# Kernel optimization log

Hardware: AMD Instinct MI355X
Metric: run time of the kernel (lower is better)

## Reference

```python
import jax, jax.numpy as jnp
import numpy as np

H = 1024      # hidden_size
NH = 16       # num_heads
HD = H // NH  # head_dim


def setup_inputs() -> dict:
    key = jax.random.key(0)
    ks = jax.random.split(key, 12)
    inp = {
        "query": jax.random.normal(ks[0], (4, 1024, H), dtype=jnp.float32),
        "key": jax.random.normal(ks[1], (4, 2048, H), dtype=jnp.float32),
        "value": jax.random.normal(ks[2], (4, 2048, H), dtype=jnp.float32),
        "key_padding_mask": jax.random.randint(ks[3], (4, 2048), 0, 2, dtype=jnp.int32),
        # learned parameters (torch Linear: y = x @ W.T + b); we store W already transposed
        "Wq": jax.random.normal(ks[4], (H, H), dtype=jnp.float32) * (1.0 / np.sqrt(H)),
        "bq": jnp.zeros((H,), dtype=jnp.float32),
        "Wk": jax.random.normal(ks[5], (H, H), dtype=jnp.float32) * (1.0 / np.sqrt(H)),
        "bk": jnp.zeros((H,), dtype=jnp.float32),
        "Wv": jax.random.normal(ks[6], (H, H), dtype=jnp.float32) * (1.0 / np.sqrt(H)),
        "bv": jnp.zeros((H,), dtype=jnp.float32),
        "Wo": jax.random.normal(ks[7], (H, H), dtype=jnp.float32) * (1.0 / np.sqrt(H)),
        "bo": jnp.zeros((H,), dtype=jnp.float32),
    }
    return inp


def reference(query, key, value, key_padding_mask, Wq, bq, Wk, bk, Wv, bv, Wo, bo):
    B, Sq, _ = query.shape
    Sk = key.shape[1]
    scaling = HD ** -0.5
    # projections -> [B, NH, S, HD]
    q = (query @ Wq + bq).reshape(B, Sq, NH, HD).transpose(0, 2, 1, 3)
    k = (key @ Wk + bk).reshape(B, Sk, NH, HD).transpose(0, 2, 1, 3)
    v = (value @ Wv + bv).reshape(B, Sk, NH, HD).transpose(0, 2, 1, 3)
    # scores [B, NH, Sq, Sk]
    scores = jnp.einsum("bhqd,bhkd->bhqk", q, k) * scaling
    # mask: positions where key_padding_mask == 0 are ignored
    scores = jnp.where((key_padding_mask == 0)[:, None, None, :], -jnp.inf, scores)
    attn = jax.nn.softmax(scores, axis=-1)
    # dropout is identity in eval mode
    out = jnp.einsum("bhqk,bhkd->bhqd", attn, v)
    out = out.transpose(0, 2, 1, 3).reshape(B, Sq, H)
    return out @ Wo + bo
```

## Files before the change

kernel.cpp:

```cpp
#include <hip/hip_runtime.h>
#include <hip/hip_fp16.h>
#include <math.h>

#define B_ 4
#define SQ 1024
#define SK 2048
#define HH 1024
#define NHEAD 16
#define HDIM 64

typedef _Float16 f16;
typedef __attribute__((ext_vector_type(8))) _Float16 f16x8;
typedef __attribute__((ext_vector_type(4))) _Float16 f16x4;
typedef __attribute__((ext_vector_type(4))) float f32x4;
typedef unsigned int u32;

#define GLOAD_LDS16(gp, lp) __builtin_amdgcn_global_load_lds( \
    (const __attribute__((address_space(1))) u32*)(gp),        \
    (__attribute__((address_space(3))) u32*)(lp), 16, 0, 0)
#define GLOAD_LDS4(gp, lp) __builtin_amdgcn_global_load_lds(  \
    (const __attribute__((address_space(1))) u32*)(gp),        \
    (__attribute__((address_space(3))) u32*)(lp), 4, 0, 0)

__global__ __launch_bounds__(256) void prep_k(
    const float* __restrict__ W0, const float* __restrict__ W1,
    const float* __restrict__ W2, const float* __restrict__ W3,
    const int* __restrict__ mask,
    f16* __restrict__ WT, float* __restrict__ pbias)
{
    __shared__ f16 t[64 * 80];
    const int bid = blockIdx.x, tid = threadIdx.x;
    if (bid < 1024) {
        int z = bid >> 8, idx = bid & 255;
        const float* W = z == 0 ? W0 : z == 1 ? W1 : z == 2 ? W2 : W3;
        f16* out = WT + (size_t)z * HH * HH;
        const int r0 = (idx >> 4) * 64, c0 = (idx & 15) * 64;
#pragma unroll
        for (int p = 0; p < 4; p++) {
            int s = p * 256 + tid;
            int row = s >> 4, u = s & 15;
            float4 a = *(const float4*)(W + (size_t)(r0 + row) * HH + c0 + u * 4);
            f16x4 vv;
            vv[0] = (f16)a.x; vv[1] = (f16)a.y; vv[2] = (f16)a.z; vv[3] = (f16)a.w;
            *(f16x4*)(t + row * 80 + u * 4) = vv;
        }
        __syncthreads();
#pragma unroll
        for (int p = 0; p < 2; p++) {
            int s = p * 256 + tid;
            int n = s >> 3, u = s & 7;
            f16x8 vv;
#pragma unroll
            for (int j = 0; j < 8; j++) vv[j] = t[(u * 8 + j) * 80 + n];
            *(f16x8*)(out + (size_t)(c0 + n) * HH + r0 + u * 8) = vv;
        }
    } else {
        int j = (bid - 1024) * 256 + tid;
        pbias[j] = mask[j] ? 0.f : -1e30f;
    }
}

template <int TM, int OUTMODE, int CASTA>
__device__ __forceinline__ void gemm_body(
    const void* Ain, const f16* __restrict__ BT,
    const float* __restrict__ bias, void* __restrict__ Cout,
    int bid, int nwg, f16* sA, f16* sB)
{
    const int tid = threadIdx.x, lane = tid & 63, w = tid >> 6;
    const int swz = (bid & 7) * (nwg >> 3) + (bid >> 3);
    const int m0 = (swz >> 3) * TM;
    const int n0 = (swz & 7) * 128;
    const int wr = w >> 1, wc = w & 1;
    const int ql = lane & 15, g = lane >> 4;
    const int N = 1024, K = 1024;
    const int MF = TM / 32;
    const int ABUF = TM * 32;
    f32x4 acc[TM / 32][4] = {};

    auto stage = [&](int buf, int k0) {
        if (CASTA) {
            const float* A32 = (const float*)Ain;
#pragma unroll
            for (int p = 0; p < TM / 64; p++) {
                int s = p * 256 + tid;
                int row = s >> 2, u = s & 3;
                const float* ap = A32 + (size_t)(m0 + row) * K + k0 + u * 8;
                float4 a0 = *(const float4*)ap;
                float4 a1 = *(const float4*)(ap + 4);
                f16x8 v;
                v[0] = (f16)a0.x; v[1] = (f16)a0.y; v[2] = (f16)a0.z; v[3] = (f16)a0.w;
                v[4] = (f16)a1.x; v[5] = (f16)a1.y; v[6] = (f16)a1.z; v[7] = (f16)a1.w;
                *(f16x8*)(sA + buf * ABUF + row * 32 + ((u ^ ((row >> 1) & 3)) * 8)) = v;
            }
        } else {
            const f16* A16 = (const f16*)Ain;
#pragma unroll
            for (int p = 0; p < TM / 64; p++) {
                int s = p * 256 + tid;
                int row = s >> 2, us = ((s & 3) ^ ((row >> 1) & 3)) * 8;
                GLOAD_LDS16(A16 + (size_t)(m0 + row) * K + k0 + us,
                            sA + buf * ABUF + (p * 256 + w * 64) * 8);
            }
        }
#pragma unroll
        for (int p = 0; p < 2; p++) {
            int s = p * 256 + tid;
            int row = s >> 2, us = ((s & 3) ^ ((row >> 1) & 3)) * 8;
            GLOAD_LDS16(BT + (size_t)(n0 + row) * K + k0 + us,
                        sB + buf * 4096 + (p * 256 + w * 64) * 8);
        }
    };

    stage(0, 0);
    int cur = 0;
    for (int k0 = 0; k0 < K; k0 += 32) {
        __syncthreads();
        if (k0 + 32 < K) stage(cur ^ 1, k0 + 32);
        f16x8 af[MF], bf[4];
#pragma unroll
        for (int m = 0; m < MF; m++) {
            int row = wr * (TM / 2) + m * 16 + ql;
            af[m] = *(const f16x8*)(sA + cur * ABUF + row * 32 + ((g ^ ((row >> 1) & 3)) * 8));
        }
#pragma unroll
        for (int n = 0; n < 4; n++) {
            int row = wc * 64 + n * 16 + ql;
            bf[n] = *(const f16x8*)(sB + cur * 4096 + row * 32 + ((g ^ ((row >> 1) & 3)) * 8));
        }
#pragma unroll
        for (int m = 0; m < MF; m++)
#pragma unroll
            for (int n = 0; n < 4; n++)
                acc[m][n] = __builtin_amdgcn_mfma_f32_16x16x32_f16(af[m], bf[n], acc[m][n], 0, 0, 0);
        cur ^= 1;
    }

    float bv[4];
#pragma unroll
    for (int n = 0; n < 4; n++) bv[n] = bias[n0 + wc * 64 + n * 16 + ql];
#pragma unroll
    for (int m = 0; m < MF; m++) {
        int row0 = m0 + wr * (TM / 2) + m * 16 + g * 4;
#pragma unroll
        for (int n = 0; n < 4; n++) {
            int col = n0 + wc * 64 + n * 16 + ql;
            if (OUTMODE == 2) {
                int bb = row0 >> 11, kk = row0 & 2047;
                int hh = col >> 6, dd = col & 63;
                f16x4 vv;
#pragma unroll
                for (int e = 0; e < 4; e++) vv[e] = (f16)(acc[m][n][e] + bv[n]);
                *(f16x4*)((f16*)Cout + ((size_t)(bb * NHEAD + hh) * HDIM + dd) * SK + kk) = vv;
            } else if (OUTMODE == 1) {
#pragma unroll
                for (int e = 0; e < 4; e++)
                    ((f16*)Cout)[(size_t)(row0 + e) * N + col] = (f16)(acc[m][n][e] + bv[n]);
            } else {
#pragma unroll
                for (int e = 0; e < 4; e++)
                    ((float*)Cout)[(size_t)(row0 + e) * N + col] = acc[m][n][e] + bv[n];
            }
        }
    }
}

__global__ __launch_bounds__(256) void qkv_gemm_k(
    const float* __restrict__ q, const float* __restrict__ k,
    const float* __restrict__ v, const f16* __restrict__ wT,
    const float* __restrict__ bq, const float* __restrict__ bk,
    const float* __restrict__ bv,
    f16* __restrict__ qp, f16* __restrict__ kp, f16* __restrict__ vt)
{
    __shared__ f16 sA[2 * 4096];
    __shared__ f16 sB[2 * 4096];
    const int bid = blockIdx.x;
    const size_t M1 = 1024 * 1024;
    if (bid < 512)
        gemm_body<64, 1, 1>(q, wT, bq, qp, bid, 512, sA, sB);
    else if (bid < 1024)
        gemm_body<128, 1, 1>(k, wT + M1, bk, kp, bid - 512, 512, sA, sB);
    else
        gemm_body<128, 2, 1>(v, wT + 2 * M1, bv, vt, bid - 1024, 512, sA, sB);
}

__global__ __launch_bounds__(256) void o_gemm_k(
    const f16* __restrict__ ctx, const f16* __restrict__ wT,
    const float* __restrict__ bo, float* __restrict__ out)
{
    __shared__ f16 sA[2 * 4096];
    __shared__ f16 sB[2 * 4096];
    gemm_body<64, 0, 0>(ctx, wT, bo, out, blockIdx.x, 512, sA, sB);
}

#define SC2 0.18033688f
#define THR2 11.5f

__global__ __launch_bounds__(512, 4) void attn_mfma_k(
    const f16* __restrict__ qp,
    const f16* __restrict__ kp,
    const f16* __restrict__ vt,
    const float* __restrict__ pbias,
    f16* __restrict__ ctx)
{
    const int flat = ((int)blockIdx.x & 7) * 64 + ((int)blockIdx.x >> 3);
    const int qt = flat & 7, h = (flat >> 3) & 15, b = flat >> 7;
    const int q0 = qt * 128;
    const int tid = threadIdx.x, lane = tid & 63, w = tid >> 6;
    const int ql = lane & 15, g = lane >> 4;

    __shared__ f16 ks[2 * 4096];
    __shared__ f16 vs[2 * 4096];
    __shared__ f16 plds[8][16 * 64];
    __shared__ float sbias[2][64];

    const f16* kbase = kp + (size_t)b * SK * HH + h * HDIM;
    const f16* vbase = vt + ((size_t)(b * NHEAD + h)) * HDIM * SK;
    const float* bbase = pbias + b * SK;

    f16x8 qf[2];
    {
        const f16* qb = qp + ((size_t)(b * SQ + q0 + w * 16 + ql)) * HH + h * HDIM + g * 8;
        qf[0] = *(const f16x8*)qb;
        qf[1] = *(const f16x8*)(qb + 32);
    }

    auto stageKV = [&](int buf, int kt) {
        int r = tid >> 3, ulg = ((tid & 7) ^ (r & 7)) * 8;
        GLOAD_LDS16(kbase + (size_t)(kt + r) * HH + ulg, ks + buf * 4096 + w * 512);
        GLOAD_LDS16(vbase + (size_t)r * SK + kt + ulg,   vs + buf * 4096 + w * 512);
        if (w == 0) GLOAD_LDS4(bbase + kt + lane, &sbias[buf][0]);
    };

    f32x4 oacc[4] = {};
    float mrun = -1e30f, lrun = 0.f;
    f16* pw = &plds[w][0];

    auto tile = [&](const f16* kb, const f16* vb, const float* sb,
                    bool pf_en, int pbuf, int pkt) {
        __syncthreads();
        if (pf_en) stageKV(pbuf, pkt);

        f32x4 sacc[4] = {};
        __builtin_amdgcn_s_setprio(1);
#pragma unroll
        for (int n = 0; n < 4; n++) {
            int key = n * 16 + ql;
#pragma unroll
            for (int df = 0; df < 2; df++) {
                int u = df * 4 + g;
                f16x8 kf = *(const f16x8*)(kb + key * 64 + ((u ^ (key & 7)) * 8));
                sacc[n] = __builtin_amdgcn_mfma_f32_16x16x32_f16(kf, qf[df], sacc[n], 0, 0, 0);
            }
        }
        __builtin_amdgcn_s_setprio(0);

        float sv[4][4];
        float mt = -1e30f;
#pragma unroll
        for (int n = 0; n < 4; n++) {
            float4 b4 = *(const float4*)&sb[n * 16 + g * 4];
            float barr[4] = {b4.x, b4.y, b4.z, b4.w};
#pragma unroll
            for (int e = 0; e < 4; e++) {
                float s = fmaf(sacc[n][e], SC2, barr[e]);
                sv[n][e] = s;
                mt = fmaxf(mt, s);
            }
        }
        mt = fmaxf(mt, __shfl_xor(mt, 16, 64));
        mt = fmaxf(mt, __shfl_xor(mt, 32, 64));

        if (__any(mt > mrun + THR2)) {
            float mnew = fmaxf(mrun, mt);
            float alpha = __builtin_amdgcn_exp2f(mrun - mnew);
            mrun = mnew;
            lrun *= alpha;
            float al[4];
#pragma unroll
            for (int e = 0; e < 4; e++) al[e] = __shfl(alpha, g * 4 + e, 64);
#pragma unroll
            for (int df = 0; df < 4; df++)
#pragma unroll
                for (int e = 0; e < 4; e++) oacc[df][e] *= al[e];
        }

        float tsum = 0.f;
#pragma unroll
        for (int n = 0; n < 4; n++) {
            float p0 = __builtin_amdgcn_exp2f(sv[n][0] - mrun);
            float p1 = __builtin_amdgcn_exp2f(sv[n][1] - mrun);
            float p2 = __builtin_amdgcn_exp2f(sv[n][2] - mrun);
            float p3 = __builtin_amdgcn_exp2f(sv[n][3] - mrun);
            tsum += (p0 + p1) + (p2 + p3);
            f16x4 pv4;
            pv4[0] = (f16)p0; pv4[1] = (f16)p1; pv4[2] = (f16)p2; pv4[3] = (f16)p3;
            *(f16x4*)(pw + ql * 64 + (((2 * n + (g >> 1)) ^ (ql & 7)) * 8) + (g & 1) * 4) = pv4;
        }
        tsum += __shfl_xor(tsum, 16, 64);
        tsum += __shfl_xor(tsum, 32, 64);
        lrun += tsum;

        __builtin_amdgcn_s_setprio(1);
#pragma unroll
        for (int t = 0; t < 2; t++) {
            f16x8 pf = *(const f16x8*)(pw + ql * 64 + (((t * 4 + g) ^ (ql & 7)) * 8));
#pragma unroll
            for (int df = 0; df < 4; df++) {
                int d = df * 16 + ql;
                int u = t * 4 + g;
                f16x8 vf = *(const f16x8*)(vb + d * 64 + ((u ^ (d & 7)) * 8));
                oacc[df] = __builtin_amdgcn_mfma_f32_16x16x32_f16(pf, vf, oacc[df], 0, 0, 0);
            }
        }
        __builtin_amdgcn_s_setprio(0);
    };

    stageKV(0, 0);
#pragma unroll 1
    for (int kt = 0; kt < SK; kt += 128) {
        tile(ks, vs, sbias[0], true, 1, kt + 64);
        tile(ks + 4096, vs + 4096, sbias[1], kt + 128 < SK, 0, kt + 128);
    }

    float linv[4];
#pragma unroll
    for (int e = 0; e < 4; e++) {
        float lv = __shfl(lrun, g * 4 + e, 64);
        linv[e] = 1.f / lv;
    }
    f16* ob = ctx + ((size_t)(b * SQ + q0 + w * 16)) * HH + h * HDIM;
#pragma unroll
    for (int df = 0; df < 4; df++)
#pragma unroll
        for (int e = 0; e < 4; e++)
            ob[(size_t)(g * 4 + e) * HH + df * 16 + ql] = (f16)(oacc[df][e] * linv[e]);
}

extern "C" void kernel_launch(void* const* d_in, const int* in_sizes, int n_in,
                              void* d_out, int out_size, void* d_ws, size_t ws_size,
                              hipStream_t stream) {
    const float* query = (const float*)d_in[0];
    const float* key   = (const float*)d_in[1];
    const float* value = (const float*)d_in[2];
    const int*   mask  = (const int*)d_in[3];
    const float* Wq = (const float*)d_in[4];
    const float* bq = (const float*)d_in[5];
    const float* Wk = (const float*)d_in[6];
    const float* bk = (const float*)d_in[7];
    const float* Wv = (const float*)d_in[8];
    const float* bv = (const float*)d_in[9];
    const float* Wo = (const float*)d_in[10];
    const float* bo = (const float*)d_in[11];
    float* out = (float*)d_out;

    const size_t M1 = 1024 * 1024;
    f16* wT    = (f16*)d_ws;
    f16* qp    = wT + 4 * M1;
    f16* kp    = qp + 4 * M1;
    f16* vt    = kp + 8 * M1;
    f16* ctx   = vt + 8 * M1;
    float* pbias = (float*)(ctx + 4 * M1);

    dim3 blk(256);

    prep_k<<<dim3(1056), blk, 0, stream>>>(Wq, Wk, Wv, Wo, mask, wT, pbias);

    qkv_gemm_k<<<dim3(1536), blk, 0, stream>>>(query, key, value, wT,
                                               bq, bk, bv, qp, kp, vt);

    attn_mfma_k<<<dim3(512), dim3(512), 0, stream>>>(qp, kp, vt, pbias, ctx);

    o_gemm_k<<<dim3(512), blk, 0, stream>>>(ctx, wT + 3 * M1, bo, out);
}
```

Before: 170.6 us.

## Software-pipeline fp32 A loads through registers in QKV projection GEMM

In the fp32-cast path, the A tile is now loaded into registers one step ahead. The fp16 convert-and-store to LDS happens after the MFMA compute, so global load latency overlaps with math instead of stalling inside the staging step. The loop is unrolled by two with explicit ping-pong buffers. A launch-bounds minimum of 3 blocks per CU is added to the QKV kernel. The extra register buffers raise register pressure, and the occupancy hint may force spills.

```diff
diff --git a/kernel.cpp b/kernel.cpp
--- a/kernel.cpp
+++ b/kernel.cpp
@@ -75,33 +75,13 @@
     const int N = 1024, K = 1024;
     const int MF = TM / 32;
     const int ABUF = TM * 32;
-    f32x4 acc[TM / 32][4] = {};
-
-    auto stage = [&](int buf, int k0) {
-        if (CASTA) {
-            const float* A32 = (const float*)Ain;
-#pragma unroll
-            for (int p = 0; p < TM / 64; p++) {
-                int s = p * 256 + tid;
-                int row = s >> 2, u = s & 3;
-                const float* ap = A32 + (size_t)(m0 + row) * K + k0 + u * 8;
-                float4 a0 = *(const float4*)ap;
-                float4 a1 = *(const float4*)(ap + 4);
-                f16x8 v;
-                v[0] = (f16)a0.x; v[1] = (f16)a0.y; v[2] = (f16)a0.z; v[3] = (f16)a0.w;
-                v[4] = (f16)a1.x; v[5] = (f16)a1.y; v[6] = (f16)a1.z; v[7] = (f16)a1.w;
-                *(f16x8*)(sA + buf * ABUF + row * 32 + ((u ^ ((row >> 1) & 3)) * 8)) = v;
-            }
-        } else {
-            const f16* A16 = (const f16*)Ain;
-#pragma unroll
-            for (int p = 0; p < TM / 64; p++) {
-                int s = p * 256 + tid;
-                int row = s >> 2, us = ((s & 3) ^ ((row >> 1) & 3)) * 8;
-                GLOAD_LDS16(A16 + (size_t)(m0 + row) * K + k0 + us,
-                            sA + buf * ABUF + (p * 256 + w * 64) * 8);
-            }
-        }
+    const int NP = TM / 64;
+    f32x4 acc[MF][4] = {};
+
+    const float* A32 = (const float*)Ain;
+    const f16*   A16 = (const f16*)Ain;
+
+    auto stageB = [&](int buf, int k0) {
 #pragma unroll
         for (int p = 0; p < 2; p++) {
             int s = p * 256 + tid;
@@ -110,29 +90,88 @@
                         sB + buf * 4096 + (p * 256 + w * 64) * 8);
         }
     };
-
-    stage(0, 0);
-    int cur = 0;
-    for (int k0 = 0; k0 < K; k0 += 32) {
-        __syncthreads();
-        if (k0 + 32 < K) stage(cur ^ 1, k0 + 32);
+    auto loadA = [&](int k0, float4* r) {
+#pragma unroll
+        for (int p = 0; p < NP; p++) {
+            int s = p * 256 + tid;
+            int row = s >> 2, u = s & 3;
+            const float* ap = A32 + (size_t)(m0 + row) * K + k0 + u * 8;
+            r[2 * p]     = *(const float4*)ap;
+            r[2 * p + 1] = *(const float4*)(ap + 4);
+        }
+    };
+    auto writeA = [&](int buf, const float4* r) {
+#pragma unroll
+        for (int p = 0; p < NP; p++) {
+            int s = p * 256 + tid;
+            int row = s >> 2, u = s & 3;
+            float4 a0 = r[2 * p], a1 = r[2 * p + 1];
+            f16x8 v;
+            v[0] = (f16)a0.x; v[1] = (f16)a0.y; v[2] = (f16)a0.z; v[3] = (f16)a0.w;
+            v[4] = (f16)a1.x; v[5] = (f16)a1.y; v[6] = (f16)a1.z; v[7] = (f16)a1.w;
+            *(f16x8*)(sA + buf * ABUF + row * 32 + ((u ^ ((row >> 1) & 3)) * 8)) = v;
+        }
+    };
+    auto stageA16 = [&](int buf, int k0) {
+#pragma unroll
+        for (int p = 0; p < NP; p++) {
+            int s = p * 256 + tid;
+            int row = s >> 2, us = ((s & 3) ^ ((row >> 1) & 3)) * 8;
+            GLOAD_LDS16(A16 + (size_t)(m0 + row) * K + k0 + us,
+                        sA + buf * ABUF + (p * 256 + w * 64) * 8);
+        }
+    };
+    auto compute = [&](int buf) {
         f16x8 af[MF], bf[4];
 #pragma unroll
         for (int m = 0; m < MF; m++) {
             int row = wr * (TM / 2) + m * 16 + ql;
-            af[m] = *(const f16x8*)(sA + cur * ABUF + row * 32 + ((g ^ ((row >> 1) & 3)) * 8));
+            af[m] = *(const f16x8*)(sA + buf * ABUF + row * 32 + ((g ^ ((row >> 1) & 3)) * 8));
         }
 #pragma unroll
         for (int n = 0; n < 4; n++) {
             int row = wc * 64 + n * 16 + ql;
-            bf[n] = *(const f16x8*)(sB + cur * 4096 + row * 32 + ((g ^ ((row >> 1) & 3)) * 8));
+            bf[n] = *(const f16x8*)(sB + buf * 4096 + row * 32 + ((g ^ ((row >> 1) & 3)) * 8));
         }
 #pragma unroll
         for (int m = 0; m < MF; m++)
 #pragma unroll
             for (int n = 0; n < 4; n++)
                 acc[m][n] = __builtin_amdgcn_mfma_f32_16x16x32_f16(af[m], bf[n], acc[m][n], 0, 0, 0);
-        cur ^= 1;
+    };
+
+    if (CASTA) {
+        float4 r0[2 * NP], r1[2 * NP];
+        loadA(0, r0);
+        stageB(0, 0);
+        writeA(0, r0);
+        loadA(32, r0);
+#pragma unroll 1
+        for (int k0 = 0; k0 < K; k0 += 64) {
+            __syncthreads();
+            stageB(1, k0 + 32);
+            if (k0 + 64 < K) loadA(k0 + 64, r1);
+            compute(0);
+            writeA(1, r0);
+            __syncthreads();
+            if (k0 + 64 < K) {
+                stageB(0, k0 + 64);
+                if (k0 + 96 < K) loadA(k0 + 96, r0);
+            }
+            compute(1);
+            if (k0 + 64 < K) writeA(0, r1);
+        }
+    } else {
+        stageA16(0, 0);
+        stageB(0, 0);
+        int cur = 0;
+#pragma unroll 1
+        for (int k0 = 0; k0 < K; k0 += 32) {
+            __syncthreads();
+            if (k0 + 32 < K) { stageA16(cur ^ 1, k0 + 32); stageB(cur ^ 1, k0 + 32); }
+            compute(cur);
+            cur ^= 1;
+        }
     }
 
     float bv[4];
@@ -164,7 +203,7 @@
     }
 }
 
-__global__ __launch_bounds__(256) void qkv_gemm_k(
+__global__ __launch_bounds__(256, 3) void qkv_gemm_k(
     const float* __restrict__ q, const float* __restrict__ k,
     const float* __restrict__ v, const f16* __restrict__ wT,
     const float* __restrict__ bq, const float* __restrict__ bk,
```

Result: faster. 154.8 us (-9.2%).
